# Kernel tuning notes

Hardware: AMD Instinct MI355X
Metric: run time of the kernel (lower is better)

## Reference

```python
import jax, jax.numpy as jnp
import numpy as np

B, L, D = 2, 2048, 1024
H = 16
HD = D // H  # 64
EPS = 1e-3  # keras GroupNormalization default epsilon


def _rotary(L_, hd, start_index=0):
    inv_freq = 1.0 / (10000.0 ** (jnp.arange(0, hd, 2, dtype=jnp.float32) / hd))
    t = jnp.arange(start_index, start_index + L_, dtype=jnp.float32)
    freqs = t[:, None] * inv_freq[None, :]          # [L, hd/2]
    emb = jnp.concatenate([freqs, freqs], axis=-1)  # [L, hd]
    return jnp.cos(emb), jnp.sin(emb)


def _rotate(x, cos, sin):
    # x: [B, H, L, hd]; cos/sin broadcast as [1, 1, L, hd]
    half = x.shape[-1] // 2
    x1, x2 = x[..., :half], x[..., half:]
    rotated = jnp.concatenate([-x2, x1], axis=-1)
    return x * cos + rotated * sin


def setup_inputs() -> dict:
    key = jax.random.key(0)
    ks = jax.random.split(key, 6)
    s = 0.02
    return {
        "inputs": jax.random.normal(ks[0], (B, L, D), dtype=jnp.float32),
        "Wq": jax.random.normal(ks[1], (D, D), dtype=jnp.float32) * s,
        "Wk": jax.random.normal(ks[2], (D, D), dtype=jnp.float32) * s,
        "Wv": jax.random.normal(ks[3], (D, D), dtype=jnp.float32) * s,
        "Wg": jax.random.normal(ks[4], (D, D), dtype=jnp.float32) * s,
        "Wo": jax.random.normal(ks[5], (D, D), dtype=jnp.float32) * s,
        "gn_gamma": jnp.ones((D,), dtype=jnp.float32),
        "gn_beta": jnp.zeros((D,), dtype=jnp.float32),
    }


def reference(inputs, Wq, Wk, Wv, Wg, Wo, gn_gamma, gn_beta):
    scaling = HD ** -0.5

    def split_heads(x):
        return x.reshape(B, L, H, HD).transpose(0, 2, 1, 3)  # [B, H, L, hd]

    q = split_heads(inputs @ Wq)
    k = split_heads(inputs @ Wk)
    v = split_heads(inputs @ Wv)

    cos, sin = _rotary(L, HD)
    cos = cos[None, None]  # [1, 1, L, hd]
    sin = sin[None, None]
    q = _rotate(q, cos, sin)
    k = _rotate(k, cos, sin)

    # decay mask: gamma_h ** (n - m) for n >= m else 0
    gammas = 1.0 - 2.0 ** (-5.0 - jnp.arange(H, dtype=jnp.float32))  # [H]
    n = jnp.arange(L, dtype=jnp.float32)
    diff = n[:, None] - n[None, :]                                    # [L, L]
    decay = jnp.where(diff >= 0, gammas[:, None, None] ** diff[None], 0.0)  # [H, L, L]

    scores = jnp.einsum('bhid,bhjd->bhij', q, k) * scaling            # [B, H, L, L]
    retention = scores * decay[None]
    out = jnp.einsum('bhij,bhjd->bhid', retention, v)                 # [B, H, L, hd]

    out = out.transpose(0, 2, 1, 3)                                   # [B, L, H, hd]
    # GroupNormalization(groups=H, axis=-1) on flattened [B*L, D]:
    # normalize over each group's hd channels per (b, l) sample
    mean = out.mean(axis=-1, keepdims=True)
    var = out.var(axis=-1, keepdims=True)
    out = (out - mean) * jax.lax.rsqrt(var + EPS)
    out = out * gn_gamma.reshape(H, HD) + gn_beta.reshape(H, HD)
    out = out.reshape(B, L, D)

    gate = jax.nn.silu(inputs @ Wg)  # swish
    return (gate * out) @ Wo
```

## Files before the change

### kernel.cpp

```cpp
#include <hip/hip_runtime.h>
#include <math.h>

typedef __attribute__((ext_vector_type(8))) short bf16x8;
typedef __attribute__((ext_vector_type(4))) float f32x4;

#define B_   2
#define L_   2048
#define D_   1024
#define H_   16
#define HD_  64
#define EPS_ 1e-3f
#define ML   (B_*L_)
#define NBIG 4096

#define MFMA(a,b,c) __builtin_amdgcn_mfma_f32_16x16x32_bf16((a),(b),(c),0,0,0)

__device__ __forceinline__ unsigned short f2bf(float f) {
    unsigned int x = __float_as_uint(f);
    x += 0x7fffu + ((x >> 16) & 1u);
    return (unsigned short)(x >> 16);
}
__device__ __forceinline__ float bf2f(unsigned short u) {
    return __uint_as_float(((unsigned int)u) << 16);
}

__global__ __launch_bounds__(256) void conv_weights(
        const float* __restrict__ W0, const float* __restrict__ W1,
        const float* __restrict__ W2, const float* __restrict__ W3,
        const float* __restrict__ W4,
        unsigned short* __restrict__ WTh, unsigned short* __restrict__ WTl) {
    __shared__ float tile[64][65];
    const int bx = blockIdx.x;
    const int w  = bx >> 8;
    const int tn = bx & 255;
    const int k0 = (tn >> 4) * 64;
    const int n0 = (tn & 15) * 64;
    const float* W = (w == 0) ? W0 : (w == 1) ? W1 : (w == 2) ? W2
                   : (w == 3) ? W3 : W4;
    const int t = threadIdx.x;
#pragma unroll
    for (int p = 0; p < 16; p++) {
        int idx = p * 256 + t;
        int r = idx >> 6, c = idx & 63;
        tile[r][c] = W[(size_t)(k0 + r) * 1024 + n0 + c];
    }
    __syncthreads();
#pragma unroll
    for (int p = 0; p < 16; p++) {
        int idx = p * 256 + t;
        int r = idx >> 6, c = idx & 63;
        float v = tile[c][r];
        size_t o = (size_t)(w * 1024 + n0 + r) * 1024 + k0 + c;
        unsigned short hb = f2bf(v);
        WTh[o] = hb;
        WTl[o] = f2bf(v - bf2f(hb));
    }
}

__global__ __launch_bounds__(256) void conv_x(const float* __restrict__ x,
        unsigned short* __restrict__ xh, unsigned short* __restrict__ xl) {
    size_t idx = (size_t)(blockIdx.x * 256 + threadIdx.x) * 4;
    float4 v = *(const float4*)&x[idx];
    ushort4 h, lo;
    h.x = f2bf(v.x); lo.x = f2bf(v.x - bf2f(h.x));
    h.y = f2bf(v.y); lo.y = f2bf(v.y - bf2f(h.y));
    h.z = f2bf(v.z); lo.z = f2bf(v.z - bf2f(h.z));
    h.w = f2bf(v.w); lo.w = f2bf(v.w - bf2f(h.w));
    *(ushort4*)&xh[idx] = h;
    *(ushort4*)&xl[idx] = lo;
}

__global__ __launch_bounds__(256) void gemm_split(
        const unsigned short* __restrict__ Ah, const unsigned short* __restrict__ Al,
        const unsigned short* __restrict__ Bh, const unsigned short* __restrict__ Bl,
        float* __restrict__ C, int M, int N, int K) {
    __shared__ unsigned short As_h[128][40], As_l[128][40];
    __shared__ unsigned short Bs_h[128][40], Bs_l[128][40];

    const int tid = threadIdx.x;
    const int l  = tid & 63;
    const int w  = tid >> 6;
    const int lg = l >> 4, lr = l & 15;
    const int wr = w >> 1, wc = w & 1;
    const int bm = blockIdx.y * 128, bn = blockIdx.x * 128;

    f32x4 acc[4][4];
#pragma unroll
    for (int mb = 0; mb < 4; mb++)
#pragma unroll
        for (int nb = 0; nb < 4; nb++) acc[mb][nb] = (f32x4){0.f, 0.f, 0.f, 0.f};

    const int srow = tid >> 1;
    const int scol = (tid & 1) * 16;

    for (int k0 = 0; k0 < K; k0 += 32) {
        const unsigned short* pAh = Ah + (size_t)(bm + srow) * K + k0 + scol;
        const unsigned short* pAl = Al + (size_t)(bm + srow) * K + k0 + scol;
        const unsigned short* pBh = Bh + (size_t)(bn + srow) * K + k0 + scol;
        const unsigned short* pBl = Bl + (size_t)(bn + srow) * K + k0 + scol;
        bf16x8 ra0 = *(const bf16x8*)pAh;       bf16x8 ra1 = *(const bf16x8*)(pAh + 8);
        bf16x8 rb0 = *(const bf16x8*)pAl;       bf16x8 rb1 = *(const bf16x8*)(pAl + 8);
        bf16x8 rc0 = *(const bf16x8*)pBh;       bf16x8 rc1 = *(const bf16x8*)(pBh + 8);
        bf16x8 rd0 = *(const bf16x8*)pBl;       bf16x8 rd1 = *(const bf16x8*)(pBl + 8);

        __syncthreads();
        *(bf16x8*)&As_h[srow][scol]     = ra0;  *(bf16x8*)&As_h[srow][scol + 8] = ra1;
        *(bf16x8*)&As_l[srow][scol]     = rb0;  *(bf16x8*)&As_l[srow][scol + 8] = rb1;
        *(bf16x8*)&Bs_h[srow][scol]     = rc0;  *(bf16x8*)&Bs_h[srow][scol + 8] = rc1;
        *(bf16x8*)&Bs_l[srow][scol]     = rd0;  *(bf16x8*)&Bs_l[srow][scol + 8] = rd1;
        __syncthreads();

        bf16x8 bh_[4], bl_[4];
#pragma unroll
        for (int nb = 0; nb < 4; nb++) {
            bh_[nb] = *(const bf16x8*)&Bs_h[wc * 64 + nb * 16 + lr][lg * 8];
            bl_[nb] = *(const bf16x8*)&Bs_l[wc * 64 + nb * 16 + lr][lg * 8];
        }
#pragma unroll
        for (int mb = 0; mb < 4; mb++) {
            bf16x8 ah_ = *(const bf16x8*)&As_h[wr * 64 + mb * 16 + lr][lg * 8];
            bf16x8 al_ = *(const bf16x8*)&As_l[wr * 64 + mb * 16 + lr][lg * 8];
#pragma unroll
            for (int nb = 0; nb < 4; nb++) {
                f32x4 a = acc[mb][nb];
                a = MFMA(ah_, bh_[nb], a);
                a = MFMA(ah_, bl_[nb], a);
                a = MFMA(al_, bh_[nb], a);
                acc[mb][nb] = a;
            }
        }
    }

#pragma unroll
    for (int mb = 0; mb < 4; mb++)
#pragma unroll
        for (int r = 0; r < 4; r++) {
            size_t row = (size_t)(bm + wr * 64 + mb * 16 + lg * 4 + r);
#pragma unroll
            for (int nb = 0; nb < 4; nb++)
                C[row * N + bn + wc * 64 + nb * 16 + lr] = acc[mb][nb][r];
        }
}

__global__ __launch_bounds__(256) void rope_inplace(float* __restrict__ QKVG) {
    int idx = blockIdx.x * 256 + threadIdx.x;
    int dd  = idx & 31;
    int h   = (idx >> 5) & (H_ - 1);
    int row = idx >> 9;
    int tp  = row & (L_ - 1);
    const float C1 = 0.41524101186092029f;
    float ang = (float)tp * exp2f(-(float)dd * C1);
    float s, c;
    sincosf(ang, &s, &c);
    size_t base = (size_t)row * NBIG;
    int cq = h * HD_ + dd;
    float q1 = QKVG[base + cq], q2 = QKVG[base + cq + 32];
    QKVG[base + cq]      = q1 * c - q2 * s;
    QKVG[base + cq + 32] = q2 * c + q1 * s;
    int ck = 1024 + cq;
    float k1 = QKVG[base + ck], k2 = QKVG[base + ck + 32];
    QKVG[base + ck]      = k1 * c - k2 * s;
    QKVG[base + ck + 32] = k2 * c + k1 * s;
}

__global__ __launch_bounds__(256) void retention_mfma(
        const float* __restrict__ QKVG,
        unsigned short* __restrict__ Yh, unsigned short* __restrict__ Yl,
        const float* __restrict__ gng, const float* __restrict__ gnb) {
    __shared__ unsigned short Ksh[64][72], Ksl[64][72];
    __shared__ unsigned short Vth[64][72], Vtl[64][72];
    __shared__ unsigned short Ssh[64][72], Ssl[64][72];

    const int qt = 31 - blockIdx.y;
    const int bh = blockIdx.x;
    const int b = bh >> 4, h = bh & (H_ - 1);
    const int tid = threadIdx.x;
    const int l = tid & 63, w = tid >> 6;
    const int lg = l >> 4, lr = l & 15;
    const int rowb = b * L_, q0 = qt * 64, hcol = h * HD_;

    const float l2g = log2f(1.f - exp2f(-(float)(5 + h)));

    float rq[4], ckf[4];
#pragma unroll
    for (int r = 0; r < 4; r++)
        rq[r] = exp2f(l2g * (float)(16 * w + lg * 4 + r));
#pragma unroll
    for (int jb = 0; jb < 4; jb++)
        ckf[jb] = exp2f(-l2g * (float)(16 * jb + lr));

    bf16x8 qh[2], ql[2];
    {
        size_t qrow = (size_t)(rowb + q0 + 16 * w + lr);
#pragma unroll
        for (int ks = 0; ks < 2; ks++) {
            const float* p = &QKVG[qrow * NBIG + hcol + ks * 32 + lg * 8];
            float4 v0 = *(const float4*)p;
            float4 v1 = *(const float4*)(p + 4);
            float vv[8] = {v0.x, v0.y, v0.z, v0.w, v1.x, v1.y, v1.z, v1.w};
            bf16x8 hh, ll;
#pragma unroll
            for (int j = 0; j < 8; j++) {
                unsigned short hb = f2bf(vv[j]);
                hh[j] = (short)hb;
                ll[j] = (short)f2bf(vv[j] - bf2f(hb));
            }
            qh[ks] = hh; ql[ks] = ll;
        }
    }

    f32x4 o4[4];
#pragma unroll
    for (int db = 0; db < 4; db++) o4[db] = (f32x4){0.f, 0.f, 0.f, 0.f};

    const int srow = tid >> 2;
    const int scb  = tid & 3;

    for (int kt = 0; kt <= qt; kt++) {
        __syncthreads();

        size_t krow = (size_t)(rowb + kt * 64 + srow) * NBIG;
        const float* pk = &QKVG[krow + 1024 + hcol + scb * 16];
        const float* pv = &QKVG[krow + 2048 + hcol + scb * 16];
#pragma unroll
        for (int half = 0; half < 2; half++) {
            float4 a = *(const float4*)(pk + half * 8);
            float4 b2 = *(const float4*)(pk + half * 8 + 4);
            float kv[8] = {a.x, a.y, a.z, a.w, b2.x, b2.y, b2.z, b2.w};
            bf16x8 hh, ll;
#pragma unroll
            for (int j = 0; j < 8; j++) {
                unsigned short hb = f2bf(kv[j]);
                hh[j] = (short)hb;
                ll[j] = (short)f2bf(kv[j] - bf2f(hb));
            }
            *(bf16x8*)&Ksh[srow][scb * 16 + half * 8] = hh;
            *(bf16x8*)&Ksl[srow][scb * 16 + half * 8] = ll;
        }
        {
            float4 a = *(const float4*)pv;
            float4 b2 = *(const float4*)(pv + 4);
            float4 c2 = *(const float4*)(pv + 8);
            float4 d2 = *(const float4*)(pv + 12);
            float vv[16] = {a.x, a.y, a.z, a.w, b2.x, b2.y, b2.z, b2.w,
                            c2.x, c2.y, c2.z, c2.w, d2.x, d2.y, d2.z, d2.w};
#pragma unroll
            for (int j = 0; j < 16; j++) {
                unsigned short hb = f2bf(vv[j]);
                Vth[scb * 16 + j][srow] = hb;
                Vtl[scb * 16 + j][srow] = f2bf(vv[j] - bf2f(hb));
            }
        }
        __syncthreads();

        float tf = 0.125f * exp2f(l2g * (float)(64 * (qt - kt)));
        float trq[4];
#pragma unroll
        for (int r = 0; r < 4; r++) trq[r] = tf * rq[r];

        const bool diag = (kt == qt);
#pragma unroll
        for (int jb = 0; jb < 4; jb++) {
            bf16x8 kh0 = *(const bf16x8*)&Ksh[16 * jb + lr][lg * 8];
            bf16x8 kh1 = *(const bf16x8*)&Ksh[16 * jb + lr][32 + lg * 8];
            bf16x8 kl0 = *(const bf16x8*)&Ksl[16 * jb + lr][lg * 8];
            bf16x8 kl1 = *(const bf16x8*)&Ksl[16 * jb + lr][32 + lg * 8];
            f32x4 s4 = (f32x4){0.f, 0.f, 0.f, 0.f};
            s4 = MFMA(qh[0], kh0, s4);
            s4 = MFMA(qh[1], kh1, s4);
            s4 = MFMA(qh[0], kl0, s4);
            s4 = MFMA(qh[1], kl1, s4);
            s4 = MFMA(ql[0], kh0, s4);
            s4 = MFMA(ql[1], kh1, s4);
#pragma unroll
            for (int r = 0; r < 4; r++) {
                float sv = s4[r] * trq[r] * ckf[jb];
                if (diag) {
                    int d = (16 * w + lg * 4 + r) - (16 * jb + lr);
                    if (d < 0) sv = 0.f;
                }
                unsigned short hb = f2bf(sv);
                Ssh[16 * w + lg * 4 + r][16 * jb + lr] = hb;
                Ssl[16 * w + lg * 4 + r][16 * jb + lr] = f2bf(sv - bf2f(hb));
            }
        }

        bf16x8 sh0 = *(const bf16x8*)&Ssh[16 * w + lr][lg * 8];
        bf16x8 sh1 = *(const bf16x8*)&Ssh[16 * w + lr][32 + lg * 8];
        bf16x8 sl0 = *(const bf16x8*)&Ssl[16 * w + lr][lg * 8];
        bf16x8 sl1 = *(const bf16x8*)&Ssl[16 * w + lr][32 + lg * 8];
#pragma unroll
        for (int db = 0; db < 4; db++) {
            bf16x8 vh0 = *(const bf16x8*)&Vth[16 * db + lr][lg * 8];
            bf16x8 vh1 = *(const bf16x8*)&Vth[16 * db + lr][32 + lg * 8];
            bf16x8 vl0 = *(const bf16x8*)&Vtl[16 * db + lr][lg * 8];
            bf16x8 vl1 = *(const bf16x8*)&Vtl[16 * db + lr][32 + lg * 8];
            f32x4 a = o4[db];
            a = MFMA(sh0, vh0, a);
            a = MFMA(sh1, vh1, a);
            a = MFMA(sh0, vl0, a);
            a = MFMA(sh1, vl1, a);
            a = MFMA(sl0, vh0, a);
            a = MFMA(sl1, vh1, a);
            o4[db] = a;
        }
    }

    float sum[4], sq[4];
#pragma unroll
    for (int r = 0; r < 4; r++) {
        float s_ = 0.f, q_ = 0.f;
#pragma unroll
        for (int db = 0; db < 4; db++) { float v = o4[db][r]; s_ += v; q_ += v * v; }
        sum[r] = s_; sq[r] = q_;
    }
#pragma unroll
    for (int m = 1; m < 16; m <<= 1) {
#pragma unroll
        for (int r = 0; r < 4; r++) {
            sum[r] += __shfl_xor(sum[r], m);
            sq[r]  += __shfl_xor(sq[r], m);
        }
    }
#pragma unroll
    for (int r = 0; r < 4; r++) {
        float mean = sum[r] * (1.f / 64.f);
        float var  = sq[r] * (1.f / 64.f) - mean * mean;
        float rstd = rsqrtf(var + EPS_);
        size_t row = (size_t)(rowb + q0 + 16 * w + lg * 4 + r);
#pragma unroll
        for (int db = 0; db < 4; db++) {
            int c = db * 16 + lr;
            float g = QKVG[row * NBIG + 3072 + hcol + c];
            float y = (o4[db][r] - mean) * rstd * gng[hcol + c] + gnb[hcol + c];
            float sig = 1.f / (1.f + expf(-g));
            float res = y * g * sig;
            unsigned short hb = f2bf(res);
            Yh[row * 1024 + hcol + c] = hb;
            Yl[row * 1024 + hcol + c] = f2bf(res - bf2f(hb));
        }
    }
}

extern "C" void kernel_launch(void* const* d_in, const int* in_sizes, int n_in,
                              void* d_out, int out_size, void* d_ws, size_t ws_size,
                              hipStream_t stream) {
    const float* x   = (const float*)d_in[0];
    const float* Wq  = (const float*)d_in[1];
    const float* Wk  = (const float*)d_in[2];
    const float* Wv  = (const float*)d_in[3];
    const float* Wg  = (const float*)d_in[4];
    const float* Wo  = (const float*)d_in[5];
    const float* gng = (const float*)d_in[6];
    const float* gnb = (const float*)d_in[7];

    char* ws = (char*)d_ws;
    float*          QKVG = (float*)ws;
    unsigned short* xh   = (unsigned short*)(ws + (size_t)64 * 1024 * 1024);
    unsigned short* xl   = (unsigned short*)(ws + (size_t)72 * 1024 * 1024);
    unsigned short* WTh  = (unsigned short*)(ws + (size_t)80 * 1024 * 1024);
    unsigned short* WTl  = (unsigned short*)(ws + (size_t)90 * 1024 * 1024);
    unsigned short* Yh   = xh;
    unsigned short* Yl   = xl;

    conv_weights<<<5 * 256, 256, 0, stream>>>(Wq, Wk, Wv, Wg, Wo, WTh, WTl);
    conv_x<<<(ML * D_) / (256 * 4), 256, 0, stream>>>(x, xh, xl);

    gemm_split<<<dim3(NBIG / 128, ML / 128), 256, 0, stream>>>(
        xh, xl, WTh, WTl, QKVG, ML, NBIG, D_);

    rope_inplace<<<(ML * H_ * (HD_ / 2)) / 256, 256, 0, stream>>>(QKVG);

    retention_mfma<<<dim3(B_ * H_, L_ / 64), 256, 0, stream>>>(
        QKVG, Yh, Yl, gng, gnb);

    gemm_split<<<dim3(D_ / 128, ML / 128), 256, 0, stream>>>(
        Yh, Yl, WTh + (size_t)4 * 1024 * 1024, WTl + (size_t)4 * 1024 * 1024,
        (float*)d_out, ML, D_, D_);
}
```

Before: 389.9 us.

## Restructure pipeline: LDS-direct GEMM, fused RoPE/split postproc, per-wave retention

The split-bf16 GEMM now stages tiles through global_load_lds with a block-swizzled grid. RoPE and the hi/lo bf16 splitting of Q/K move into a postproc kernel that writes packed bf16 pairs and a transposed V. The retention kernel becomes wave-granular with balanced causal work pairing, reading K directly from global memory. A new 64-row output GEMM consumes the packed gated output. Together these aim to remove repeated fp32→bf16 conversions, LDS staging overhead and load imbalance, at the cost of extra buffer passes and more complex aliasing of the workspace.

```diff
diff --git a/kernel.cpp b/kernel.cpp
--- a/kernel.cpp
+++ b/kernel.cpp
@@ -12,16 +12,29 @@
 #define EPS_ 1e-3f
 #define ML   (B_*L_)
 #define NBIG 4096
+#define PU   8192
+
+#define OQ(h)  ((h) * 128)
+#define OK_(h) (2048 + (h) * 128)
+#define OY(h)  (4096 + (h) * 128)
 
 #define MFMA(a,b,c) __builtin_amdgcn_mfma_f32_16x16x32_bf16((a),(b),(c),0,0,0)
 
-__device__ __forceinline__ unsigned short f2bf(float f) {
-    unsigned int x = __float_as_uint(f);
-    x += 0x7fffu + ((x >> 16) & 1u);
-    return (unsigned short)(x >> 16);
-}
-__device__ __forceinline__ float bf2f(unsigned short u) {
-    return __uint_as_float(((unsigned int)u) << 16);
+__device__ __forceinline__ void rsplit(float f, unsigned short& hi, unsigned short& lo) {
+    unsigned int u = __float_as_uint(f);
+    unsigned int r = u + (0x7fffu + ((u >> 16) & 1u));
+    hi = (unsigned short)(r >> 16);
+    float fh = __uint_as_float((unsigned int)(r & 0xffff0000u));
+    float fl = f - fh;
+    unsigned int ul = __float_as_uint(fl);
+    unsigned int rl = ul + (0x7fffu + ((ul >> 16) & 1u));
+    lo = (unsigned short)(rl >> 16);
+}
+
+__device__ __forceinline__ void gload16(const unsigned short* src, unsigned short* lds) {
+    __builtin_amdgcn_global_load_lds(
+        (const __attribute__((address_space(1))) unsigned int*)src,
+        (__attribute__((address_space(3))) unsigned int*)lds, 16, 0, 0);
 }
 
 __global__ __launch_bounds__(256) void conv_weights(
@@ -51,9 +64,9 @@
         int r = idx >> 6, c = idx & 63;
         float v = tile[c][r];
         size_t o = (size_t)(w * 1024 + n0 + r) * 1024 + k0 + c;
-        unsigned short hb = f2bf(v);
-        WTh[o] = hb;
-        WTl[o] = f2bf(v - bf2f(hb));
+        unsigned short hb, lb;
+        rsplit(v, hb, lb);
+        WTh[o] = hb; WTl[o] = lb;
     }
 }
 
@@ -62,284 +75,393 @@
     size_t idx = (size_t)(blockIdx.x * 256 + threadIdx.x) * 4;
     float4 v = *(const float4*)&x[idx];
     ushort4 h, lo;
-    h.x = f2bf(v.x); lo.x = f2bf(v.x - bf2f(h.x));
-    h.y = f2bf(v.y); lo.y = f2bf(v.y - bf2f(h.y));
-    h.z = f2bf(v.z); lo.z = f2bf(v.z - bf2f(h.z));
-    h.w = f2bf(v.w); lo.w = f2bf(v.w - bf2f(h.w));
+    rsplit(v.x, h.x, lo.x); rsplit(v.y, h.y, lo.y);
+    rsplit(v.z, h.z, lo.z); rsplit(v.w, h.w, lo.w);
     *(ushort4*)&xh[idx] = h;
     *(ushort4*)&xl[idx] = lo;
 }
 
-__global__ __launch_bounds__(256) void gemm_split(
+__global__ __launch_bounds__(256) void gemm_ldst(
         const unsigned short* __restrict__ Ah, const unsigned short* __restrict__ Al,
         const unsigned short* __restrict__ Bh, const unsigned short* __restrict__ Bl,
-        float* __restrict__ C, int M, int N, int K) {
-    __shared__ unsigned short As_h[128][40], As_l[128][40];
-    __shared__ unsigned short Bs_h[128][40], Bs_l[128][40];
-
-    const int tid = threadIdx.x;
-    const int l  = tid & 63;
-    const int w  = tid >> 6;
-    const int lg = l >> 4, lr = l & 15;
-    const int wr = w >> 1, wc = w & 1;
-    const int bm = blockIdx.y * 128, bn = blockIdx.x * 128;
-
-    f32x4 acc[4][4];
-#pragma unroll
-    for (int mb = 0; mb < 4; mb++)
-#pragma unroll
-        for (int nb = 0; nb < 4; nb++) acc[mb][nb] = (f32x4){0.f, 0.f, 0.f, 0.f};
-
-    const int srow = tid >> 1;
-    const int scol = (tid & 1) * 16;
-
-    for (int k0 = 0; k0 < K; k0 += 32) {
-        const unsigned short* pAh = Ah + (size_t)(bm + srow) * K + k0 + scol;
-        const unsigned short* pAl = Al + (size_t)(bm + srow) * K + k0 + scol;
-        const unsigned short* pBh = Bh + (size_t)(bn + srow) * K + k0 + scol;
-        const unsigned short* pBl = Bl + (size_t)(bn + srow) * K + k0 + scol;
-        bf16x8 ra0 = *(const bf16x8*)pAh;       bf16x8 ra1 = *(const bf16x8*)(pAh + 8);
-        bf16x8 rb0 = *(const bf16x8*)pAl;       bf16x8 rb1 = *(const bf16x8*)(pAl + 8);
-        bf16x8 rc0 = *(const bf16x8*)pBh;       bf16x8 rc1 = *(const bf16x8*)(pBh + 8);
-        bf16x8 rd0 = *(const bf16x8*)pBl;       bf16x8 rd1 = *(const bf16x8*)(pBl + 8);
-
-        __syncthreads();
-        *(bf16x8*)&As_h[srow][scol]     = ra0;  *(bf16x8*)&As_h[srow][scol + 8] = ra1;
-        *(bf16x8*)&As_l[srow][scol]     = rb0;  *(bf16x8*)&As_l[srow][scol + 8] = rb1;
-        *(bf16x8*)&Bs_h[srow][scol]     = rc0;  *(bf16x8*)&Bs_h[srow][scol + 8] = rc1;
-        *(bf16x8*)&Bs_l[srow][scol]     = rd0;  *(bf16x8*)&Bs_l[srow][scol + 8] = rd1;
-        __syncthreads();
-
-        bf16x8 bh_[4], bl_[4];
-#pragma unroll
-        for (int nb = 0; nb < 4; nb++) {
-            bh_[nb] = *(const bf16x8*)&Bs_h[wc * 64 + nb * 16 + lr][lg * 8];
-            bl_[nb] = *(const bf16x8*)&Bs_l[wc * 64 + nb * 16 + lr][lg * 8];
-        }
-#pragma unroll
-        for (int mb = 0; mb < 4; mb++) {
-            bf16x8 ah_ = *(const bf16x8*)&As_h[wr * 64 + mb * 16 + lr][lg * 8];
-            bf16x8 al_ = *(const bf16x8*)&As_l[wr * 64 + mb * 16 + lr][lg * 8];
-#pragma unroll
-            for (int nb = 0; nb < 4; nb++) {
-                f32x4 a = acc[mb][nb];
-                a = MFMA(ah_, bh_[nb], a);
-                a = MFMA(ah_, bl_[nb], a);
-                a = MFMA(al_, bh_[nb], a);
-                acc[mb][nb] = a;
-            }
-        }
-    }
-
-#pragma unroll
-    for (int mb = 0; mb < 4; mb++)
-#pragma unroll
-        for (int r = 0; r < 4; r++) {
-            size_t row = (size_t)(bm + wr * 64 + mb * 16 + lg * 4 + r);
-#pragma unroll
-            for (int nb = 0; nb < 4; nb++)
-                C[row * N + bn + wc * 64 + nb * 16 + lr] = acc[mb][nb][r];
-        }
-}
-
-__global__ __launch_bounds__(256) void rope_inplace(float* __restrict__ QKVG) {
-    int idx = blockIdx.x * 256 + threadIdx.x;
-    int dd  = idx & 31;
-    int h   = (idx >> 5) & (H_ - 1);
-    int row = idx >> 9;
-    int tp  = row & (L_ - 1);
-    const float C1 = 0.41524101186092029f;
-    float ang = (float)tp * exp2f(-(float)dd * C1);
-    float s, c;
-    sincosf(ang, &s, &c);
-    size_t base = (size_t)row * NBIG;
-    int cq = h * HD_ + dd;
-    float q1 = QKVG[base + cq], q2 = QKVG[base + cq + 32];
-    QKVG[base + cq]      = q1 * c - q2 * s;
-    QKVG[base + cq + 32] = q2 * c + q1 * s;
-    int ck = 1024 + cq;
-    float k1 = QKVG[base + ck], k2 = QKVG[base + ck + 32];
-    QKVG[base + ck]      = k1 * c - k2 * s;
-    QKVG[base + ck + 32] = k2 * c + k1 * s;
-}
-
-__global__ __launch_bounds__(256) void retention_mfma(
-        const float* __restrict__ QKVG,
-        unsigned short* __restrict__ Yh, unsigned short* __restrict__ Yl,
-        const float* __restrict__ gng, const float* __restrict__ gnb) {
-    __shared__ unsigned short Ksh[64][72], Ksl[64][72];
-    __shared__ unsigned short Vth[64][72], Vtl[64][72];
-    __shared__ unsigned short Ssh[64][72], Ssl[64][72];
-
-    const int qt = 31 - blockIdx.y;
-    const int bh = blockIdx.x;
-    const int b = bh >> 4, h = bh & (H_ - 1);
+        float* __restrict__ C, int M, int N, int K, int gx) {
+    __shared__ unsigned short SMEM[4][128 * 32];
+
     const int tid = threadIdx.x;
     const int l = tid & 63, w = tid >> 6;
     const int lg = l >> 4, lr = l & 15;
-    const int rowb = b * L_, q0 = qt * 64, hcol = h * HD_;
-
+    const int wr = w >> 1, wc = w & 1;
+
+    const int cpx = gridDim.x >> 3;
+    const int flat = blockIdx.x;
+    const int swz = (flat & 7) * cpx + (flat >> 3);
+    const int bm = (swz / gx) * 128, bn = (swz % gx) * 128;
+
+    const unsigned short* arr = (w == 0) ? Ah : (w == 1) ? Al : (w == 2) ? Bh : Bl;
+    const int rbase = (w < 2) ? bm : bn;
+    const unsigned short* src0 = arr + (size_t)(rbase + (l >> 2)) * K + (l & 3) * 8;
+
+    f32x4 acc[4][4];
+#pragma unroll
+    for (int mb = 0; mb < 4; mb++)
+#pragma unroll
+        for (int nb = 0; nb < 4; nb++) acc[mb][nb] = (f32x4){0.f, 0.f, 0.f, 0.f};
+
+    for (int k0 = 0; k0 < K; k0 += 32) {
+        __syncthreads();
+#pragma unroll
+        for (int i = 0; i < 8; i++)
+            gload16(src0 + (size_t)i * 16 * K + k0, &SMEM[w][i * 512]);
+        __syncthreads();
+
+        bf16x8 bhf[4], blf[4];
+#pragma unroll
+        for (int nb = 0; nb < 4; nb++) {
+            bhf[nb] = *(const bf16x8*)&SMEM[2][(wc * 64 + nb * 16 + lr) * 32 + lg * 8];
+            blf[nb] = *(const bf16x8*)&SMEM[3][(wc * 64 + nb * 16 + lr) * 32 + lg * 8];
+        }
+#pragma unroll
+        for (int mb = 0; mb < 4; mb++) {
+            bf16x8 ahf = *(const bf16x8*)&SMEM[0][(wr * 64 + mb * 16 + lr) * 32 + lg * 8];
+            bf16x8 alf = *(const bf16x8*)&SMEM[1][(wr * 64 + mb * 16 + lr) * 32 + lg * 8];
+#pragma unroll
+            for (int nb = 0; nb < 4; nb++) {
+                f32x4 a = acc[mb][nb];
+                a = MFMA(ahf, bhf[nb], a);
+                a = MFMA(ahf, blf[nb], a);
+                a = MFMA(alf, bhf[nb], a);
+                acc[mb][nb] = a;
+            }
+        }
+    }
+
+#pragma unroll
+    for (int mb = 0; mb < 4; mb++)
+#pragma unroll
+        for (int r = 0; r < 4; r++) {
+            size_t row = (size_t)(bm + wr * 64 + mb * 16 + lg * 4 + r);
+#pragma unroll
+            for (int nb = 0; nb < 4; nb++)
+                C[row * N + bn + wc * 64 + nb * 16 + lr] = acc[mb][nb][r];
+        }
+}
+
+__global__ __launch_bounds__(256) void postproc(float* __restrict__ QKVG,
+        unsigned short* __restrict__ Vth, unsigned short* __restrict__ Vtl) {
+    __shared__ float T[64][65];
+    const int bid = blockIdx.x;
+    const int bh = bid >> 5, st = bid & 31;
+    const int b = bh >> 4, h = bh & (H_ - 1);
+    const int t = threadIdx.x;
+    const int row0 = b * L_ + st * 64;
+    const int hcol = h * HD_;
+    unsigned short* U = (unsigned short*)QKVG;
+
+    const int seq = t >> 2;
+    const int dd0 = (t & 3) * 8;
+
+    {
+        const int cb = (t & 3) * 16;
+        const float* p = QKVG + (size_t)(row0 + seq) * NBIG + 2048 + hcol + cb;
+#pragma unroll
+        for (int f = 0; f < 4; f++) {
+            float4 v = *(const float4*)(p + f * 4);
+            T[cb + f * 4 + 0][seq] = v.x;
+            T[cb + f * 4 + 1][seq] = v.y;
+            T[cb + f * 4 + 2][seq] = v.z;
+            T[cb + f * 4 + 3][seq] = v.w;
+        }
+    }
+
+    float qo1[8], qo2[8], ko1[8], ko2[8];
+    {
+        const float* pq = QKVG + (size_t)(row0 + seq) * NBIG + hcol;
+        const float* pk = pq + 1024;
+        float4 qa = *(const float4*)(pq + dd0);      float4 qb = *(const float4*)(pq + dd0 + 4);
+        float4 qc = *(const float4*)(pq + dd0 + 32); float4 qd = *(const float4*)(pq + dd0 + 36);
+        float4 ka = *(const float4*)(pk + dd0);      float4 kb = *(const float4*)(pk + dd0 + 4);
+        float4 kc = *(const float4*)(pk + dd0 + 32); float4 kd = *(const float4*)(pk + dd0 + 36);
+        float q1[8] = {qa.x,qa.y,qa.z,qa.w, qb.x,qb.y,qb.z,qb.w};
+        float q2[8] = {qc.x,qc.y,qc.z,qc.w, qd.x,qd.y,qd.z,qd.w};
+        float k1[8] = {ka.x,ka.y,ka.z,ka.w, kb.x,kb.y,kb.z,kb.w};
+        float k2[8] = {kc.x,kc.y,kc.z,kc.w, kd.x,kd.y,kd.z,kd.w};
+        const float C1 = 0.41524101186092029f;
+        const int tp = st * 64 + seq;
+#pragma unroll
+        for (int j = 0; j < 8; j++) {
+            float ang = (float)tp * exp2f(-(float)(dd0 + j) * C1);
+            float s_, c_;
+            sincosf(ang, &s_, &c_);
+            qo1[j] = q1[j] * c_ - q2[j] * s_;  qo2[j] = q2[j] * c_ + q1[j] * s_;
+            ko1[j] = k1[j] * c_ - k2[j] * s_;  ko2[j] = k2[j] * c_ + k1[j] * s_;
+        }
+    }
+    __syncthreads();
+
+    {
+        const int d = t >> 2, sb = (t & 3) * 16;
+        bf16x8 hv[2], lv[2];
+#pragma unroll
+        for (int f = 0; f < 16; f++) {
+            unsigned short hb, lb;
+            rsplit(T[d][sb + f], hb, lb);
+            hv[f >> 3][f & 7] = (short)hb;
+            lv[f >> 3][f & 7] = (short)lb;
+        }
+        size_t o = ((size_t)bh * HD_ + d) * L_ + st * 64 + sb;
+        *(bf16x8*)&Vth[o] = hv[0]; *(bf16x8*)&Vth[o + 8] = hv[1];
+        *(bf16x8*)&Vtl[o] = lv[0]; *(bf16x8*)&Vtl[o + 8] = lv[1];
+    }
+
+    {
+        size_t rb = (size_t)(row0 + seq) * PU;
+        bf16x8 v_[8];
+#pragma unroll
+        for (int j = 0; j < 8; j++) {
+            unsigned short hb, lb;
+            rsplit(qo1[j], hb, lb); v_[0][j] = (short)hb; v_[1][j] = (short)lb;
+            rsplit(qo2[j], hb, lb); v_[2][j] = (short)hb; v_[3][j] = (short)lb;
+            rsplit(ko1[j], hb, lb); v_[4][j] = (short)hb; v_[5][j] = (short)lb;
+            rsplit(ko2[j], hb, lb); v_[6][j] = (short)hb; v_[7][j] = (short)lb;
+        }
+        *(bf16x8*)&U[rb + OQ(h)  + dd0]       = v_[0];
+        *(bf16x8*)&U[rb + OQ(h)  + 64 + dd0]  = v_[1];
+        *(bf16x8*)&U[rb + OQ(h)  + 32 + dd0]  = v_[2];
+        *(bf16x8*)&U[rb + OQ(h)  + 96 + dd0]  = v_[3];
+        *(bf16x8*)&U[rb + OK_(h) + dd0]       = v_[4];
+        *(bf16x8*)&U[rb + OK_(h) + 64 + dd0]  = v_[5];
+        *(bf16x8*)&U[rb + OK_(h) + 32 + dd0]  = v_[6];
+        *(bf16x8*)&U[rb + OK_(h) + 96 + dd0]  = v_[7];
+    }
+}
+
+__global__ __launch_bounds__(256) void retention_v3(
+        float* __restrict__ QKVG,
+        const unsigned short* __restrict__ Vth, const unsigned short* __restrict__ Vtl,
+        const float* __restrict__ gng, const float* __restrict__ gnb) {
+    __shared__ unsigned short Ssh[4][16][72];
+    __shared__ unsigned short Ssl[4][16][72];
+
+    unsigned short* U = (unsigned short*)QKVG;
+    const int tid = threadIdx.x;
+    const int w = tid >> 6, l = tid & 63;
+    const int lg = l >> 4, lr = l & 15;
+
+    const int bsw = ((blockIdx.x & 7) << 6) | (blockIdx.x >> 3);
+    const int g = bsw * 4 + w;
+    const int bh = g >> 6;
+    const int ps = g & 63;
+    const int b = bh >> 4, h = bh & (H_ - 1);
+    const size_t rowb = (size_t)b * L_;
+    const int hcol = h * HD_;
     const float l2g = log2f(1.f - exp2f(-(float)(5 + h)));
 
-    float rq[4], ckf[4];
-#pragma unroll
-    for (int r = 0; r < 4; r++)
-        rq[r] = exp2f(l2g * (float)(16 * w + lg * 4 + r));
+    float cfl[4];
 #pragma unroll
     for (int jb = 0; jb < 4; jb++)
-        ckf[jb] = exp2f(-l2g * (float)(16 * jb + lr));
-
-    bf16x8 qh[2], ql[2];
-    {
-        size_t qrow = (size_t)(rowb + q0 + 16 * w + lr);
-#pragma unroll
-        for (int ks = 0; ks < 2; ks++) {
-            const float* p = &QKVG[qrow * NBIG + hcol + ks * 32 + lg * 8];
-            float4 v0 = *(const float4*)p;
-            float4 v1 = *(const float4*)(p + 4);
-            float vv[8] = {v0.x, v0.y, v0.z, v0.w, v1.x, v1.y, v1.z, v1.w};
-            bf16x8 hh, ll;
-#pragma unroll
-            for (int j = 0; j < 8; j++) {
-                unsigned short hb = f2bf(vv[j]);
-                hh[j] = (short)hb;
-                ll[j] = (short)f2bf(vv[j] - bf2f(hb));
-            }
-            qh[ks] = hh; ql[ks] = ll;
-        }
-    }
-
-    f32x4 o4[4];
-#pragma unroll
-    for (int db = 0; db < 4; db++) o4[db] = (f32x4){0.f, 0.f, 0.f, 0.f};
-
-    const int srow = tid >> 2;
-    const int scb  = tid & 3;
-
-    for (int kt = 0; kt <= qt; kt++) {
+        cfl[jb] = exp2f(-l2g * (float)(16 * jb + lr));
+
+#pragma unroll 1
+    for (int half = 0; half < 2; half++) {
+        const int s = half ? (127 - ps) : ps;
+        const int rowq = s * 16;
+        const int ktiles = (s >> 2) + 1;
+
+        float rq[4];
+#pragma unroll
+        for (int r = 0; r < 4; r++)
+            rq[r] = 0.125f * exp2f(l2g * (float)(rowq + lg * 4 + r));
+
+        bf16x8 qfh[2], qfl[2];
+        {
+            size_t qo = (rowb + rowq + lr) * PU + OQ(h);
+            qfh[0] = *(const bf16x8*)&U[qo + lg * 8];
+            qfh[1] = *(const bf16x8*)&U[qo + 32 + lg * 8];
+            qfl[0] = *(const bf16x8*)&U[qo + 64 + lg * 8];
+            qfl[1] = *(const bf16x8*)&U[qo + 96 + lg * 8];
+        }
+
+        f32x4 o4[4];
+#pragma unroll
+        for (int db = 0; db < 4; db++) o4[db] = (f32x4){0.f, 0.f, 0.f, 0.f};
+
+        for (int kt = 0; kt < ktiles; kt++) {
+            const float ckt = exp2f(-l2g * (float)(kt * 64));
+            float rqt[4];
+#pragma unroll
+            for (int r = 0; r < 4; r++) rqt[r] = rq[r] * ckt;
+            const bool lastt = (kt == ktiles - 1);
+
+            f32x4 s4[4];
+#pragma unroll
+            for (int jb = 0; jb < 4; jb++) {
+                size_t ko = (rowb + kt * 64 + jb * 16 + lr) * PU + OK_(h);
+                bf16x8 k0h = *(const bf16x8*)&U[ko + lg * 8];
+                bf16x8 k1h = *(const bf16x8*)&U[ko + 32 + lg * 8];
+                bf16x8 k0l = *(const bf16x8*)&U[ko + 64 + lg * 8];
+                bf16x8 k1l = *(const bf16x8*)&U[ko + 96 + lg * 8];
+                f32x4 sv = (f32x4){0.f, 0.f, 0.f, 0.f};
+                sv = MFMA(qfh[0], k0h, sv);
+                sv = MFMA(qfh[1], k1h, sv);
+                sv = MFMA(qfh[0], k0l, sv);
+                sv = MFMA(qfh[1], k1l, sv);
+                sv = MFMA(qfl[0], k0h, sv);
+                sv = MFMA(qfl[1], k1h, sv);
+                s4[jb] = sv;
+            }
+
+#pragma unroll
+            for (int jb = 0; jb < 4; jb++) {
+#pragma unroll
+                for (int r = 0; r < 4; r++) {
+                    float sv = s4[jb][r] * rqt[r] * cfl[jb];
+                    if (lastt) {
+                        int qi = rowq + lg * 4 + r;
+                        int kj = kt * 64 + jb * 16 + lr;
+                        sv = (kj > qi) ? 0.f : sv;
+                    }
+                    unsigned short sh_, sl_;
+                    rsplit(sv, sh_, sl_);
+                    Ssh[w][lg * 4 + r][jb * 16 + lr] = sh_;
+                    Ssl[w][lg * 4 + r][jb * 16 + lr] = sl_;
+                }
+            }
+
+            bf16x8 sfh[2], sfl[2];
+            sfh[0] = *(const bf16x8*)&Ssh[w][lr][lg * 8];
+            sfh[1] = *(const bf16x8*)&Ssh[w][lr][32 + lg * 8];
+            sfl[0] = *(const bf16x8*)&Ssl[w][lr][lg * 8];
+            sfl[1] = *(const bf16x8*)&Ssl[w][lr][32 + lg * 8];
+#pragma unroll
+            for (int db = 0; db < 4; db++) {
+                size_t vo = ((size_t)bh * HD_ + db * 16 + lr) * L_ + kt * 64;
+                bf16x8 v0h = *(const bf16x8*)&Vth[vo + lg * 8];
+                bf16x8 v1h = *(const bf16x8*)&Vth[vo + 32 + lg * 8];
+                bf16x8 v0l = *(const bf16x8*)&Vtl[vo + lg * 8];
+                bf16x8 v1l = *(const bf16x8*)&Vtl[vo + 32 + lg * 8];
+                f32x4 a = o4[db];
+                a = MFMA(sfh[0], v0h, a);
+                a = MFMA(sfh[1], v1h, a);
+                a = MFMA(sfh[0], v0l, a);
+                a = MFMA(sfh[1], v1l, a);
+                a = MFMA(sfl[0], v0h, a);
+                a = MFMA(sfl[1], v1h, a);
+                o4[db] = a;
+            }
+        }
+
+        float sum_[4], sq_[4];
+#pragma unroll
+        for (int r = 0; r < 4; r++) {
+            float s_ = 0.f, q_ = 0.f;
+#pragma unroll
+            for (int db = 0; db < 4; db++) { float v = o4[db][r]; s_ += v; q_ += v * v; }
+            sum_[r] = s_; sq_[r] = q_;
+        }
+#pragma unroll
+        for (int m = 1; m < 16; m <<= 1) {
+#pragma unroll
+            for (int r = 0; r < 4; r++) {
+                sum_[r] += __shfl_xor(sum_[r], m, 64);
+                sq_[r]  += __shfl_xor(sq_[r], m, 64);
+            }
+        }
+#pragma unroll
+        for (int r = 0; r < 4; r++) {
+            float mean = sum_[r] * (1.f / 64.f);
+            float var  = sq_[r] * (1.f / 64.f) - mean * mean;
+            float rstd = rsqrtf(var + EPS_);
+            size_t row = rowb + rowq + lg * 4 + r;
+#pragma unroll
+            for (int db = 0; db < 4; db++) {
+                int c = db * 16 + lr;
+                float gv = QKVG[row * NBIG + 3072 + hcol + c];
+                float y = (o4[db][r] - mean) * rstd * gng[hcol + c] + gnb[hcol + c];
+                float sig = 1.f / (1.f + expf(-gv));
+                float res = y * gv * sig;
+                unsigned short hb, lb;
+                rsplit(res, hb, lb);
+                U[row * PU + OY(h) + c]      = hb;
+                U[row * PU + OY(h) + 64 + c] = lb;
+            }
+        }
+    }
+}
+
+__global__ __launch_bounds__(256) void gemm_out64(
+        const unsigned short* __restrict__ U,
+        const unsigned short* __restrict__ Bh, const unsigned short* __restrict__ Bl,
+        float* __restrict__ C) {
+    __shared__ unsigned short As_h[64][40], As_l[64][40];
+    __shared__ unsigned short Bs_h[128][40], Bs_l[128][40];
+    const int K = 1024, N = 1024;
+
+    const int tid = threadIdx.x;
+    const int l = tid & 63, w = tid >> 6;
+    const int lg = l >> 4, lr = l & 15;
+    const int wr = w >> 1, wc = w & 1;
+
+    const int flat = blockIdx.x;
+    const int swz = (flat & 7) * 64 + (flat >> 3);
+    const int bm = (swz >> 3) * 64, bn = (swz & 7) * 128;
+
+    f32x4 acc[2][4];
+#pragma unroll
+    for (int mb = 0; mb < 2; mb++)
+#pragma unroll
+        for (int nb = 0; nb < 4; nb++) acc[mb][nb] = (f32x4){0.f, 0.f, 0.f, 0.f};
+
+    const int arow = tid >> 2, acol = (tid & 3) * 8;
+    const int brow = tid >> 1, bcol = (tid & 1) * 16;
+
+    for (int k0 = 0; k0 < K; k0 += 32) {
+        const int e0 = k0 + acol;
+        const size_t aoff = (size_t)(bm + arow) * PU + 4096
+                          + ((e0 >> 6) << 7) + (e0 & 63);
+        bf16x8 a_h = *(const bf16x8*)&U[aoff];
+        bf16x8 a_l = *(const bf16x8*)&U[aoff + 64];
+        bf16x8 b_h0 = *(const bf16x8*)&Bh[(size_t)(bn + brow) * K + k0 + bcol];
+        bf16x8 b_h1 = *(const bf16x8*)&Bh[(size_t)(bn + brow) * K + k0 + bcol + 8];
+        bf16x8 b_l0 = *(const bf16x8*)&Bl[(size_t)(bn + brow) * K + k0 + bcol];
+        bf16x8 b_l1 = *(const bf16x8*)&Bl[(size_t)(bn + brow) * K + k0 + bcol + 8];
+
         __syncthreads();
-
-        size_t krow = (size_t)(rowb + kt * 64 + srow) * NBIG;
-        const float* pk = &QKVG[krow + 1024 + hcol + scb * 16];
-        const float* pv = &QKVG[krow + 2048 + hcol + scb * 16];
-#pragma unroll
-        for (int half = 0; half < 2; half++) {
-            float4 a = *(const float4*)(pk + half * 8);
-            float4 b2 = *(const float4*)(pk + half * 8 + 4);
-            float kv[8] = {a.x, a.y, a.z, a.w, b2.x, b2.y, b2.z, b2.w};
-            bf16x8 hh, ll;
-#pragma unroll
-            for (int j = 0; j < 8; j++) {
-                unsigned short hb = f2bf(kv[j]);
-                hh[j] = (short)hb;
-                ll[j] = (short)f2bf(kv[j] - bf2f(hb));
-            }
-            *(bf16x8*)&Ksh[srow][scb * 16 + half * 8] = hh;
-            *(bf16x8*)&Ksl[srow][scb * 16 + half * 8] = ll;
-        }
-        {
-            float4 a = *(const float4*)pv;
-            float4 b2 = *(const float4*)(pv + 4);
-            float4 c2 = *(const float4*)(pv + 8);
-            float4 d2 = *(const float4*)(pv + 12);
-            float vv[16] = {a.x, a.y, a.z, a.w, b2.x, b2.y, b2.z, b2.w,
-                            c2.x, c2.y, c2.z, c2.w, d2.x, d2.y, d2.z, d2.w};
-#pragma unroll
-            for (int j = 0; j < 16; j++) {
-                unsigned short hb = f2bf(vv[j]);
-                Vth[scb * 16 + j][srow] = hb;
-                Vtl[scb * 16 + j][srow] = f2bf(vv[j] - bf2f(hb));
-            }
-        }
+        *(bf16x8*)&As_h[arow][acol] = a_h;
+        *(bf16x8*)&As_l[arow][acol] = a_l;
+        *(bf16x8*)&Bs_h[brow][bcol] = b_h0; *(bf16x8*)&Bs_h[brow][bcol + 8] = b_h1;
+        *(bf16x8*)&Bs_l[brow][bcol] = b_l0; *(bf16x8*)&Bs_l[brow][bcol + 8] = b_l1;
         __syncthreads();
 
-        float tf = 0.125f * exp2f(l2g * (float)(64 * (qt - kt)));
-        float trq[4];
-#pragma unroll
-        for (int r = 0; r < 4; r++) trq[r] = tf * rq[r];
-
-        const bool diag = (kt == qt);
-#pragma unroll
-        for (int jb = 0; jb < 4; jb++) {
-            bf16x8 kh0 = *(const bf16x8*)&Ksh[16 * jb + lr][lg * 8];
-            bf16x8 kh1 = *(const bf16x8*)&Ksh[16 * jb + lr][32 + lg * 8];
-            bf16x8 kl0 = *(const bf16x8*)&Ksl[16 * jb + lr][lg * 8];
-            bf16x8 kl1 = *(const bf16x8*)&Ksl[16 * jb + lr][32 + lg * 8];
-            f32x4 s4 = (f32x4){0.f, 0.f, 0.f, 0.f};
-            s4 = MFMA(qh[0], kh0, s4);
-            s4 = MFMA(qh[1], kh1, s4);
-            s4 = MFMA(qh[0], kl0, s4);
-            s4 = MFMA(qh[1], kl1, s4);
-            s4 = MFMA(ql[0], kh0, s4);
-            s4 = MFMA(ql[1], kh1, s4);
-#pragma unroll
-            for (int r = 0; r < 4; r++) {
-                float sv = s4[r] * trq[r] * ckf[jb];
-                if (diag) {
-                    int d = (16 * w + lg * 4 + r) - (16 * jb + lr);
-                    if (d < 0) sv = 0.f;
-                }
-                unsigned short hb = f2bf(sv);
-                Ssh[16 * w + lg * 4 + r][16 * jb + lr] = hb;
-                Ssl[16 * w + lg * 4 + r][16 * jb + lr] = f2bf(sv - bf2f(hb));
-            }
-        }
-
-        bf16x8 sh0 = *(const bf16x8*)&Ssh[16 * w + lr][lg * 8];
-        bf16x8 sh1 = *(const bf16x8*)&Ssh[16 * w + lr][32 + lg * 8];
-        bf16x8 sl0 = *(const bf16x8*)&Ssl[16 * w + lr][lg * 8];
-        bf16x8 sl1 = *(const bf16x8*)&Ssl[16 * w + lr][32 + lg * 8];
-#pragma unroll
-        for (int db = 0; db < 4; db++) {
-            bf16x8 vh0 = *(const bf16x8*)&Vth[16 * db + lr][lg * 8];
-            bf16x8 vh1 = *(const bf16x8*)&Vth[16 * db + lr][32 + lg * 8];
-            bf16x8 vl0 = *(const bf16x8*)&Vtl[16 * db + lr][lg * 8];
-            bf16x8 vl1 = *(const bf16x8*)&Vtl[16 * db + lr][32 + lg * 8];
-            f32x4 a = o4[db];
-            a = MFMA(sh0, vh0, a);
-            a = MFMA(sh1, vh1, a);
-            a = MFMA(sh0, vl0, a);
-            a = MFMA(sh1, vl1, a);
-            a = MFMA(sl0, vh0, a);
-            a = MFMA(sl1, vh1, a);
-            o4[db] = a;
-        }
-    }
-
-    float sum[4], sq[4];
-#pragma unroll
-    for (int r = 0; r < 4; r++) {
-        float s_ = 0.f, q_ = 0.f;
-#pragma unroll
-        for (int db = 0; db < 4; db++) { float v = o4[db][r]; s_ += v; q_ += v * v; }
-        sum[r] = s_; sq[r] = q_;
-    }
-#pragma unroll
-    for (int m = 1; m < 16; m <<= 1) {
+        bf16x8 bhf[4], blf[4];
+#pragma unroll
+        for (int nb = 0; nb < 4; nb++) {
+            bhf[nb] = *(const bf16x8*)&Bs_h[wc * 64 + nb * 16 + lr][lg * 8];
+            blf[nb] = *(const bf16x8*)&Bs_l[wc * 64 + nb * 16 + lr][lg * 8];
+        }
+#pragma unroll
+        for (int mb = 0; mb < 2; mb++) {
+            bf16x8 ahf = *(const bf16x8*)&As_h[wr * 32 + mb * 16 + lr][lg * 8];
+            bf16x8 alf = *(const bf16x8*)&As_l[wr * 32 + mb * 16 + lr][lg * 8];
+#pragma unroll
+            for (int nb = 0; nb < 4; nb++) {
+                f32x4 a = acc[mb][nb];
+                a = MFMA(ahf, bhf[nb], a);
+                a = MFMA(ahf, blf[nb], a);
+                a = MFMA(alf, bhf[nb], a);
+                acc[mb][nb] = a;
+            }
+        }
+    }
+
+#pragma unroll
+    for (int mb = 0; mb < 2; mb++)
 #pragma unroll
         for (int r = 0; r < 4; r++) {
-            sum[r] += __shfl_xor(sum[r], m);
-            sq[r]  += __shfl_xor(sq[r], m);
-        }
-    }
-#pragma unroll
-    for (int r = 0; r < 4; r++) {
-        float mean = sum[r] * (1.f / 64.f);
-        float var  = sq[r] * (1.f / 64.f) - mean * mean;
-        float rstd = rsqrtf(var + EPS_);
-        size_t row = (size_t)(rowb + q0 + 16 * w + lg * 4 + r);
-#pragma unroll
-        for (int db = 0; db < 4; db++) {
-            int c = db * 16 + lr;
-            float g = QKVG[row * NBIG + 3072 + hcol + c];
-            float y = (o4[db][r] - mean) * rstd * gng[hcol + c] + gnb[hcol + c];
-            float sig = 1.f / (1.f + expf(-g));
-            float res = y * g * sig;
-            unsigned short hb = f2bf(res);
-            Yh[row * 1024 + hcol + c] = hb;
-            Yl[row * 1024 + hcol + c] = f2bf(res - bf2f(hb));
-        }
-    }
+            size_t row = (size_t)(bm + wr * 32 + mb * 16 + lg * 4 + r);
+#pragma unroll
+            for (int nb = 0; nb < 4; nb++)
+                C[row * N + bn + wc * 64 + nb * 16 + lr] = acc[mb][nb][r];
+        }
 }
 
 extern "C" void kernel_launch(void* const* d_in, const int* in_sizes, int n_in,
@@ -355,26 +477,24 @@
     const float* gnb = (const float*)d_in[7];
 
     char* ws = (char*)d_ws;
+    const size_t MB = 1024 * 1024;
     float*          QKVG = (float*)ws;
-    unsigned short* xh   = (unsigned short*)(ws + (size_t)64 * 1024 * 1024);
-    unsigned short* xl   = (unsigned short*)(ws + (size_t)72 * 1024 * 1024);
-    unsigned short* WTh  = (unsigned short*)(ws + (size_t)80 * 1024 * 1024);
-    unsigned short* WTl  = (unsigned short*)(ws + (size_t)90 * 1024 * 1024);
-    unsigned short* Yh   = xh;
-    unsigned short* Yl   = xl;
+    unsigned short* WTh  = (unsigned short*)(ws + (size_t)64 * MB);
+    unsigned short* WTl  = (unsigned short*)(ws + (size_t)74 * MB);
+    unsigned short* Vth  = (unsigned short*)(ws + (size_t)84 * MB);
+    unsigned short* Vtl  = (unsigned short*)(ws + (size_t)92 * MB);
+    unsigned short* U    = (unsigned short*)QKVG;
 
     conv_weights<<<5 * 256, 256, 0, stream>>>(Wq, Wk, Wv, Wg, Wo, WTh, WTl);
-    conv_x<<<(ML * D_) / (256 * 4), 256, 0, stream>>>(x, xh, xl);
-
-    gemm_split<<<dim3(NBIG / 128, ML / 128), 256, 0, stream>>>(
-        xh, xl, WTh, WTl, QKVG, ML, NBIG, D_);
-
-    rope_inplace<<<(ML * H_ * (HD_ / 2)) / 256, 256, 0, stream>>>(QKVG);
-
-    retention_mfma<<<dim3(B_ * H_, L_ / 64), 256, 0, stream>>>(
-        QKVG, Yh, Yl, gng, gnb);
-
-    gemm_split<<<dim3(D_ / 128, ML / 128), 256, 0, stream>>>(
-        Yh, Yl, WTh + (size_t)4 * 1024 * 1024, WTl + (size_t)4 * 1024 * 1024,
-        (float*)d_out, ML, D_, D_);
-}
+    conv_x<<<(ML * D_) / (256 * 4), 256, 0, stream>>>(x, Vth , Vtl );
+
+    gemm_ldst<<<1024, 256, 0, stream>>>(Vth, Vtl, WTh, WTl, QKVG, ML, NBIG, D_, 32);
+
+    postproc<<<1024, 256, 0, stream>>>(QKVG, Vth, Vtl);
+
+    retention_v3<<<512, 256, 0, stream>>>(QKVG, Vth, Vtl, gng, gnb);
+
+    gemm_out64<<<512, 256, 0, stream>>>(U,
+        WTh + (size_t)4 * 1024 * 1024, WTl + (size_t)4 * 1024 * 1024,
+        (float*)d_out);
+}
```

New measurement: 497.9 us. +27.7%, slower.
